# Performance work log

Measured on AMD Instinct MI355X. Metric: run time of the kernel, lower is better.

The kernel has to match this reference:

```python
import jax, jax.numpy as jnp
import numpy as np

H = 16  # n_heads

def _rmsnorm(x, g, eps=1e-6):
    return x * jax.lax.rsqrt(jnp.mean(x * x, axis=-1, keepdims=True) + eps) * g

def _rope_diag(L, hd, dtype):
    # Diagonal of the full [L, hd, hd] rotary matrix: cos(pos * theta_pair) at every dim.
    # (The torch einsum 'bhld,ldd->bhld' extracts this diagonal, so no pairwise rotation occurs.)
    pair = jnp.arange(hd) // 2
    theta = 10000.0 ** (-2.0 * pair / hd)
    return jnp.cos(jnp.arange(L)[:, None].astype(jnp.float32) * theta[None, :]).astype(dtype)


def setup_inputs() -> dict:
    key = jax.random.key(0)
    ks = jax.random.split(key, 8)
    B, L, E = 2, 2048, 2048
    F = 2 * E  # SwiGLU width
    s = 0.02
    return {
        "x": jax.random.normal(ks[0], (B, L, E), jnp.float32),
        "g": jnp.ones((E,), jnp.float32),
        "wq": jax.random.normal(ks[1], (E, E), jnp.float32) * s,
        "wk": jax.random.normal(ks[2], (E, E), jnp.float32) * s,
        "wv": jax.random.normal(ks[3], (E, E), jnp.float32) * s,
        "w1": jax.random.normal(ks[4], (E, F), jnp.float32) * s,
        "b1": jnp.zeros((F,), jnp.float32),
        "wg": jax.random.normal(ks[5], (F, F), jnp.float32) * s,
        "bg": jnp.zeros((F,), jnp.float32),
        "wl": jax.random.normal(ks[6], (F, F), jnp.float32) * s,
        "bl": jnp.zeros((F,), jnp.float32),
        "beta": jnp.ones((1,), jnp.float32),
        "w2": jax.random.normal(ks[7], (F, E), jnp.float32) * s,
        "b2": jnp.zeros((E,), jnp.float32),
    }


def reference(x, g, wq, wk, wv, w1, b1, wg, bg, wl, bl, beta, w2, b2):
    B, L, E = x.shape
    hd = E // H
    x_res = x
    h = _rmsnorm(x, g)
    # projections -> [B, H, L, hd]
    q = (h @ wq).reshape(B, L, H, hd).transpose(0, 2, 1, 3)
    k = (h @ wk).reshape(B, L, H, hd).transpose(0, 2, 1, 3)
    v = (h @ wv).reshape(B, L, H, hd).transpose(0, 2, 1, 3)
    D = _rope_diag(L, hd, x.dtype)  # [L, hd], diagonal of rotary matrix
    q = q * D
    k = k * D
    score = jnp.einsum('bhld,bhmd->bhlm', q, k)  # [B,H,L,L]
    # causal mask added BEFORE scaling (faithful to source)
    mask = jnp.triu(jnp.full((L, L), -jnp.inf, dtype=score.dtype), k=1)
    score = (score + mask) / jnp.sqrt(jnp.asarray(hd, score.dtype))
    attn = jax.nn.softmax(score, axis=-1)
    o = jnp.einsum('bhlm,bhmd->bhld', attn, v)
    o = o.transpose(0, 2, 1, 3).reshape(B, L, E)
    x = o + x_res
    x_res = x
    h = _rmsnorm(x, g)
    h = h @ w1 + b1  # [B, L, 2E]
    gate = h @ wg + bg
    lin = h @ wl + bl
    act = gate * jax.nn.sigmoid(beta * gate) * lin
    out = act @ w2 + b2
    return out + x_res
```

## Files before the change

kernel.cpp:

```cpp
#include <hip/hip_runtime.h>
#include <cstdint>
#include <math.h>


typedef _Float16 f16;
typedef _Float16 f16x8 __attribute__((ext_vector_type(8)));
typedef _Float16 f16x4 __attribute__((ext_vector_type(4)));
typedef float    f32x4 __attribute__((ext_vector_type(4)));

#define MFMA_16x16x32(a, b, c) __builtin_amdgcn_mfma_f32_16x16x32_f16(a, b, c, 0, 0, 0)

__device__ __forceinline__ void gload_lds16(const void* g, void* lds) {
  __builtin_amdgcn_global_load_lds(
      (__attribute__((address_space(1))) void*)(uintptr_t)g,
      (__attribute__((address_space(3))) void*)(unsigned)(uintptr_t)lds,
      16, 0, 0);
}

__global__ void convT_k(const float* __restrict__ W, f16* __restrict__ Wt,
                        int K, int N) {
  __shared__ float tile[32][33];
  const int n0 = blockIdx.x << 5, k0 = blockIdx.y << 5;
  const int t = threadIdx.x;
  const int r = t >> 3, c4 = (t & 7) << 2;
  const f32x4 v = *(const f32x4*)(W + (size_t)(k0 + r) * N + n0 + c4);
  tile[r][c4 + 0] = v[0]; tile[r][c4 + 1] = v[1];
  tile[r][c4 + 2] = v[2]; tile[r][c4 + 3] = v[3];
  __syncthreads();
  f16x4 o;
  o[0] = (f16)tile[c4 + 0][r]; o[1] = (f16)tile[c4 + 1][r];
  o[2] = (f16)tile[c4 + 2][r]; o[3] = (f16)tile[c4 + 3][r];
  *(f16x4*)(Wt + (size_t)(n0 + r) * K + k0 + c4) = o;
}

__global__ void rope_tab_k(float* __restrict__ Dt) {
  const int l = blockIdx.x, d = threadIdx.x;
  const float th = __expf(-0.0719557841f * (float)(d & ~1));
  Dt[(l << 7) + d] = cosf((float)l * th);
}

__global__ void rmsnorm_k(const float* __restrict__ X, const float* __restrict__ G,
                          f16* __restrict__ H) {
  __shared__ float red[4];
  const int row = blockIdx.x, t = threadIdx.x;
  const float* xp = X + ((size_t)row << 11) + (t << 3);
  const f32x4 v0 = *(const f32x4*)xp;
  const f32x4 v1 = *(const f32x4*)(xp + 4);
  float ss = v0[0]*v0[0] + v0[1]*v0[1] + v0[2]*v0[2] + v0[3]*v0[3]
           + v1[0]*v1[0] + v1[1]*v1[1] + v1[2]*v1[2] + v1[3]*v1[3];
#pragma unroll
  for (int m = 1; m < 64; m <<= 1) ss += __shfl_xor(ss, m);
  if ((t & 63) == 0) red[t >> 6] = ss;
  __syncthreads();
  const float tot = red[0] + red[1] + red[2] + red[3];
  const float rs = rsqrtf(tot * (1.f / 2048.f) + 1e-6f);
  const float* gp = G + (t << 3);
  const f32x4 g0 = *(const f32x4*)gp, g1 = *(const f32x4*)(gp + 4);
  f16x8 o;
  o[0] = (f16)(v0[0]*rs*g0[0]); o[1] = (f16)(v0[1]*rs*g0[1]);
  o[2] = (f16)(v0[2]*rs*g0[2]); o[3] = (f16)(v0[3]*rs*g0[3]);
  o[4] = (f16)(v1[0]*rs*g1[0]); o[5] = (f16)(v1[1]*rs*g1[1]);
  o[6] = (f16)(v1[2]*rs*g1[2]); o[7] = (f16)(v1[3]*rs*g1[3]);
  *(f16x8*)(H + ((size_t)row << 11) + (t << 3)) = o;
}

__global__ void vtrans_k(const f16* __restrict__ V, f16* __restrict__ Vt) {
  __shared__ f16 tile[32][36];
  const int l0 = blockIdx.x << 5, d0 = blockIdx.y << 5, bh = blockIdx.z;
  const int b = bh >> 4, h = bh & 15;
  const int t = threadIdx.x;
  const int r = t >> 3, c4 = (t & 7) << 2;
  const f16x4 v = *(const f16x4*)(V + (size_t)((b << 11) + l0 + r) * 2048 + (h << 7) + d0 + c4);
  tile[r][c4 + 0] = v[0]; tile[r][c4 + 1] = v[1];
  tile[r][c4 + 2] = v[2]; tile[r][c4 + 3] = v[3];
  __syncthreads();
  f16x4 o;
  o[0] = tile[c4 + 0][r]; o[1] = tile[c4 + 1][r];
  o[2] = tile[c4 + 2][r]; o[3] = tile[c4 + 3][r];
  *(f16x4*)(Vt + (size_t)((bh << 7) + d0 + r) * 2048 + l0 + c4) = o;
}

template <int EPI>
__launch_bounds__(512, 2)
__global__ void gemm256_k(const f16* __restrict__ A, const f16* __restrict__ Bt,
                          void* __restrict__ Cout, int M, int N, int K,
                          const float* __restrict__ bias,
                          const f16* __restrict__ auxh,
                          const float* __restrict__ betap) {
  __shared__ alignas(16) f16 lds[65536];
  const int t = threadIdx.x, lane = t & 63, w = t >> 6;
  const int wm = w >> 2, wn = w & 3;
  const int bm = blockIdx.y << 8, bn = blockIdx.x << 8;
  const int lh = lane & 15, lq = lane >> 4;
  const int NT = K >> 6;
  const int lrow = lane >> 3;
  const int lco  = ((lane & 7) ^ lrow) << 3;

  const f16* Agl = A  + (size_t)(bm + lrow) * K + lco;
  const f16* Bgl = Bt + (size_t)(bn + lrow) * K + lco;
  const int aw = w << 3;
  const int bw = w << 4;

  f32x4 acc[8][4] = {};
  f16x8 bf[4][2];

  auto stA = [&](int tile, int half) {
    const int d = (tile & 1) << 15;
    const int k0 = tile << 6;
    const int r0 = aw + (half << 6);
    gload_lds16(Agl + (size_t)r0 * K + k0, (void*)&lds[d + r0 * 64]);
    gload_lds16(Agl + (size_t)(r0 + 128) * K + k0, (void*)&lds[d + (r0 + 128) * 64]);
  };
  auto stB = [&](int tile, int half) {
    const int d = ((tile & 1) << 15) + 16384;
    const int k0 = tile << 6;
    const int r0 = bw + (half << 7);
    gload_lds16(Bgl + (size_t)r0 * K + k0, (void*)&lds[d + r0 * 64]);
    gload_lds16(Bgl + (size_t)(r0 + 8) * K + k0, (void*)&lds[d + (r0 + 8) * 64]);
  };
  auto ldA = [&](int d, int mi, int kk) {
    const int r = (wm << 7) + (mi << 4) + lh;
    return *(const f16x8*)&lds[(d << 15) + r * 64 + ((((kk << 2) + lq) ^ (lh & 7)) << 3)];
  };
  auto ldB = [&](int d, int ni, int kk) {
    const int r = (wn << 6) + (ni << 4) + lh;
    return *(const f16x8*)&lds[(d << 15) + 16384 + r * 64 + ((((kk << 2) + lq) ^ (lh & 7)) << 3)];
  };

  stB(0, 0); stB(0, 1); stA(0, 0); stA(0, 1);
  stB(1, 0); stB(1, 1); stA(1, 0);
  asm volatile("s_waitcnt vmcnt(6)" ::: "memory");
  __builtin_amdgcn_s_barrier();

  for (int tt = 0; tt < NT; tt += 2) {
    const bool pf = (tt + 2 < NT);
#pragma unroll
    for (int hf = 0; hf < 2; ++hf) {
#pragma unroll
      for (int ph = 0; ph < 4; ++ph) {
        f16x8 a0k0 = ldA(hf, 2 * ph, 0),     a0k1 = ldA(hf, 2 * ph, 1);
        f16x8 a1k0 = ldA(hf, 2 * ph + 1, 0), a1k1 = ldA(hf, 2 * ph + 1, 1);
        if (ph == 0) {
#pragma unroll
          for (int ni = 0; ni < 4; ++ni) {
            bf[ni][0] = ldB(hf, ni, 0); bf[ni][1] = ldB(hf, ni, 1);
          }
        }
        if (hf == 0) {
          if (ph == 0) stA(tt + 1, 1);
          else if (ph == 1) { if (pf) stB(tt + 2, 0); }
          else if (ph == 2) { if (pf) stB(tt + 2, 1); }
          else              { if (pf) stA(tt + 2, 0); }
        } else {
          if (ph == 0)      { if (pf) stA(tt + 2, 1); }
          else if (ph == 1) { if (pf) stB(tt + 3, 0); }
          else if (ph == 2) { if (pf) stB(tt + 3, 1); }
          else              { if (pf) stA(tt + 3, 0); }
        }
        __builtin_amdgcn_s_barrier();
        __builtin_amdgcn_s_setprio(1);
#pragma unroll
        for (int ni = 0; ni < 4; ++ni) {
          acc[2 * ph][ni]     = MFMA_16x16x32(a0k0, bf[ni][0], acc[2 * ph][ni]);
          acc[2 * ph][ni]     = MFMA_16x16x32(a0k1, bf[ni][1], acc[2 * ph][ni]);
          acc[2 * ph + 1][ni] = MFMA_16x16x32(a1k0, bf[ni][0], acc[2 * ph + 1][ni]);
          acc[2 * ph + 1][ni] = MFMA_16x16x32(a1k1, bf[ni][1], acc[2 * ph + 1][ni]);
        }
        __builtin_amdgcn_s_setprio(0);
        if (ph == 3) {
          if (hf == 0) {
            if (pf) asm volatile("s_waitcnt vmcnt(6)" ::: "memory");
            else    asm volatile("s_waitcnt vmcnt(0)" ::: "memory");
          } else if (pf) {
            asm volatile("s_waitcnt vmcnt(6)" ::: "memory");
          }
        }
        __builtin_amdgcn_s_barrier();
      }
    }
  }

  const float be = (EPI == 3) ? betap[0] : 0.f;
#pragma unroll
  for (int mi = 0; mi < 8; ++mi) {
#pragma unroll
    for (int ni = 0; ni < 4; ++ni) {
#pragma unroll
      for (int r = 0; r < 4; ++r) {
        const int grow = bm + (wm << 7) + (mi << 4) + (lq << 2) + r;
        const int gcol = bn + (wn << 6) + (ni << 4) + lh;
        float v = acc[mi][ni][r] + bias[gcol];
        const size_t off = (size_t)grow * N + gcol;
        if (EPI == 2) {
          ((f16*)Cout)[off] = (f16)v;
        } else if (EPI == 3) {
          ((f16*)Cout)[off] = (f16)(v / (1.f + __expf(-be * v)));
        } else {
          ((f16*)Cout)[off] = (f16)(v * (float)auxh[off]);
        }
      }
    }
  }
}

template <int EPI>
__launch_bounds__(256, 2)
__global__ void gemm_k(const f16* __restrict__ A, const f16* __restrict__ Bt,
                       void* __restrict__ Cout, int M, int N, int K,
                       const float* __restrict__ bias,
                       const float* __restrict__ auxf,
                       float scale) {
  __shared__ alignas(16) f16 As[128 * 64];
  __shared__ alignas(16) f16 Bs[128 * 64];
  const int t = threadIdx.x;
  const int lane = t & 63;
  const int w = t >> 6;
  const int wm = w >> 1, wn = w & 1;
  const int bm = blockIdx.y << 7;
  const int bn = blockIdx.x << 7;
  const int lh = lane & 15, lq = lane >> 4;

  f32x4 acc[4][4] = {};

  for (int k0 = 0; k0 < K; k0 += 64) {
    __syncthreads();
#pragma unroll
    for (int i = 0; i < 4; ++i) {
      const int idx = i * 256 + (w << 6) + lane;
      const int row = idx >> 3, c = idx & 7;
      const int cs = (c ^ (row & 7)) << 3;
      gload_lds16(A + (size_t)(bm + row) * K + k0 + cs,
                  &As[(i * 256 + (w << 6)) << 3]);
      gload_lds16(Bt + (size_t)(bn + row) * K + k0 + cs,
                  &Bs[(i * 256 + (w << 6)) << 3]);
    }
    asm volatile("s_waitcnt vmcnt(0)" ::: "memory");
    __syncthreads();
#pragma unroll
    for (int kk = 0; kk < 2; ++kk) {
      f16x8 af[4], bfr[4];
#pragma unroll
      for (int mi = 0; mi < 4; ++mi) {
        const int r = (wm << 6) + (mi << 4) + lh;
        af[mi] = *(const f16x8*)&As[(r << 6) + ((((kk << 2) + lq) ^ (r & 7)) << 3)];
      }
#pragma unroll
      for (int ni = 0; ni < 4; ++ni) {
        const int r = (wn << 6) + (ni << 4) + lh;
        bfr[ni] = *(const f16x8*)&Bs[(r << 6) + ((((kk << 2) + lq) ^ (r & 7)) << 3)];
      }
#pragma unroll
      for (int mi = 0; mi < 4; ++mi)
#pragma unroll
        for (int ni = 0; ni < 4; ++ni)
          acc[mi][ni] = MFMA_16x16x32(af[mi], bfr[ni], acc[mi][ni]);
    }
  }

#pragma unroll
  for (int mi = 0; mi < 4; ++mi) {
#pragma unroll
    for (int ni = 0; ni < 4; ++ni) {
#pragma unroll
      for (int r = 0; r < 4; ++r) {
        const int grow = bm + (wm << 6) + (mi << 4) + (lq << 2) + r;
        const int gcol = bn + (wn << 6) + (ni << 4) + lh;
        float v = acc[mi][ni][r];
        const size_t off = (size_t)grow * N + gcol;
        if (EPI == 0) {
          v *= scale * auxf[((grow & 2047) << 7) + (gcol & 127)];
          ((f16*)Cout)[off] = (f16)v;
        } else if (EPI == 1) {
          ((f16*)Cout)[off] = (f16)v;
        } else {
          ((float*)Cout)[off] = v + bias[gcol] + auxf[off];
        }
      }
    }
  }
}

__launch_bounds__(256, 2)
__global__ void attn_k(const f16* __restrict__ Q, const f16* __restrict__ Kb,
                       const f16* __restrict__ Vt, const float* __restrict__ Xres,
                       float* __restrict__ X2, int* __restrict__ qcnt) {
  constexpr int L = 2048, E = 2048, HD = 128;
  __shared__ alignas(16) f16 Ks[64 * 128];
  __shared__ alignas(16) f16 Vs[128 * 64];
  __shared__ alignas(16) f16 Ps[4][32 * 72];
  __shared__ int s_item;

  const int t = threadIdx.x, lane = t & 63, w = t >> 6;
  const int lh = lane & 15, lq = lane >> 4;

  for (;;) {
    if (t == 0) s_item = atomicAdd(qcnt, 1);
    __syncthreads();
    const int item = s_item;
    if (item >= 512) return;
    const int bh = item & 31;
    const int q0 = (15 - (item >> 5)) << 7;
    const int b = bh >> 4, h = bh & 15;
    const int wrow0 = q0 + (w << 5);

    f16x8 qf[2][4];
#pragma unroll
    for (int mi = 0; mi < 2; ++mi) {
      const f16* qrow = Q + (size_t)(b * L + wrow0 + (mi << 4) + lh) * E + h * HD;
#pragma unroll
      for (int kq = 0; kq < 4; ++kq)
        qf[mi][kq] = *(const f16x8*)(qrow + (kq << 5) + (lq << 3));
    }

    f32x4 oacc[2][8] = {};
    float mrun[2][4], lrun[2][4];
#pragma unroll
    for (int mi = 0; mi < 2; ++mi)
#pragma unroll
      for (int r = 0; r < 4; ++r) { mrun[mi][r] = -1e30f; lrun[mi][r] = 0.f; }

    const int nkv = q0 + 128;
    for (int kv0 = 0; kv0 < nkv; kv0 += 64) {
      __syncthreads();
#pragma unroll
      for (int i = 0; i < 4; ++i) {
        const int idx = i * 256 + (w << 6) + lane;
        {
          const int row = idx >> 4, c = idx & 15;
          gload_lds16(Kb + (size_t)(b * L + kv0 + row) * E + h * HD + ((c ^ (row & 7)) << 3),
                      &Ks[(i * 256 + (w << 6)) << 3]);
        }
        {
          const int row = idx >> 3, c = idx & 7;
          gload_lds16(Vt + ((size_t)bh * HD + row) * L + kv0 + ((c ^ (row & 7)) << 3),
                      &Vs[(i * 256 + (w << 6)) << 3]);
        }
      }
      asm volatile("s_waitcnt vmcnt(0)" ::: "memory");
      __syncthreads();

      if (kv0 <= wrow0 + 31) {
        f32x4 sacc[2][4] = {};
#pragma unroll
        for (int kq = 0; kq < 4; ++kq) {
          f16x8 kf[4];
#pragma unroll
          for (int ni = 0; ni < 4; ++ni) {
            const int r = (ni << 4) + lh;
            kf[ni] = *(const f16x8*)&Ks[(r << 7) + ((((kq << 2) + lq) ^ (r & 7)) << 3)];
          }
#pragma unroll
          for (int mi = 0; mi < 2; ++mi)
#pragma unroll
            for (int ni = 0; ni < 4; ++ni)
              sacc[mi][ni] = MFMA_16x16x32(qf[mi][kq], kf[ni], sacc[mi][ni]);
        }
        if (kv0 + 63 > wrow0) {
#pragma unroll
          for (int mi = 0; mi < 2; ++mi)
#pragma unroll
            for (int ni = 0; ni < 4; ++ni)
#pragma unroll
              for (int r = 0; r < 4; ++r) {
                const int qr = wrow0 + (mi << 4) + (lq << 2) + r;
                const int kv = kv0 + (ni << 4) + lh;
                if (kv > qr) sacc[mi][ni][r] = -1e30f;
              }
        }
        float scl[2][4], rsum[2][4];
#pragma unroll
        for (int mi = 0; mi < 2; ++mi)
#pragma unroll
          for (int r = 0; r < 4; ++r) {
            float v = fmaxf(fmaxf(sacc[mi][0][r], sacc[mi][1][r]),
                            fmaxf(sacc[mi][2][r], sacc[mi][3][r]));
            v = fmaxf(v, __shfl_xor(v, 1));
            v = fmaxf(v, __shfl_xor(v, 2));
            v = fmaxf(v, __shfl_xor(v, 4));
            v = fmaxf(v, __shfl_xor(v, 8));
            const float mnew = fmaxf(mrun[mi][r], v);
            scl[mi][r] = __expf(mrun[mi][r] - mnew);
            mrun[mi][r] = mnew;
            rsum[mi][r] = 0.f;
          }
#pragma unroll
        for (int mi = 0; mi < 2; ++mi)
#pragma unroll
          for (int ni = 0; ni < 4; ++ni)
#pragma unroll
            for (int r = 0; r < 4; ++r) {
              const float p = __expf(sacc[mi][ni][r] - mrun[mi][r]);
              rsum[mi][r] += p;
              Ps[w][((mi << 4) + (lq << 2) + r) * 72 + (ni << 4) + lh] = (f16)p;
            }
#pragma unroll
        for (int mi = 0; mi < 2; ++mi)
#pragma unroll
          for (int r = 0; r < 4; ++r) {
            float s = rsum[mi][r];
            s += __shfl_xor(s, 1);
            s += __shfl_xor(s, 2);
            s += __shfl_xor(s, 4);
            s += __shfl_xor(s, 8);
            lrun[mi][r] = lrun[mi][r] * scl[mi][r] + s;
          }
#pragma unroll
        for (int mi = 0; mi < 2; ++mi)
#pragma unroll
          for (int nd = 0; nd < 8; ++nd)
#pragma unroll
            for (int r = 0; r < 4; ++r) oacc[mi][nd][r] *= scl[mi][r];
#pragma unroll
        for (int kp = 0; kp < 2; ++kp) {
          f16x8 pf[2];
#pragma unroll
          for (int mi = 0; mi < 2; ++mi)
            pf[mi] = *(const f16x8*)&Ps[w][((mi << 4) + lh) * 72 + (kp << 5) + (lq << 3)];
#pragma unroll
          for (int nd = 0; nd < 8; ++nd) {
            const int r = (nd << 4) + lh;
            const f16x8 vf = *(const f16x8*)&Vs[(r << 6) + ((((kp << 2) + lq) ^ (r & 7)) << 3)];
#pragma unroll
            for (int mi = 0; mi < 2; ++mi)
              oacc[mi][nd] = MFMA_16x16x32(pf[mi], vf, oacc[mi][nd]);
          }
        }
      }
    }
#pragma unroll
    for (int mi = 0; mi < 2; ++mi)
#pragma unroll
      for (int nd = 0; nd < 8; ++nd)
#pragma unroll
        for (int r = 0; r < 4; ++r) {
          const int qr = wrow0 + (mi << 4) + (lq << 2) + r;
          const size_t off = (size_t)(b * L + qr) * E + h * HD + (nd << 4) + lh;
          X2[off] = oacc[mi][nd][r] / lrun[mi][r] + Xres[off];
        }
  }
}

extern "C" void kernel_launch(void* const* d_in, const int* in_sizes, int n_in,
                              void* d_out, int out_size, void* d_ws, size_t ws_size,
                              hipStream_t stream) {
  const float* x    = (const float*)d_in[0];
  const float* g    = (const float*)d_in[1];
  const float* wq   = (const float*)d_in[2];
  const float* wk   = (const float*)d_in[3];
  const float* wv   = (const float*)d_in[4];
  const float* w1   = (const float*)d_in[5];
  const float* b1   = (const float*)d_in[6];
  const float* wgp  = (const float*)d_in[7];
  const float* bg   = (const float*)d_in[8];
  const float* wl   = (const float*)d_in[9];
  const float* bl   = (const float*)d_in[10];
  const float* beta = (const float*)d_in[11];
  const float* w2   = (const float*)d_in[12];
  const float* b2   = (const float*)d_in[13];

  constexpr size_t MB = 1ull << 20;
  char* ws = (char*)d_ws;
  f16*   wT   = (f16*)(ws + 0 * MB);
  int*   qcnt = (int*)(ws + 31 * MB);
  float* Dt   = (float*)(ws + 32 * MB);
  f16*   hbuf = (f16*)(ws + 33 * MB);
  f16*   qbuf = (f16*)(ws + 49 * MB);
  f16*   kbuf = (f16*)(ws + 65 * MB);
  f16*   vbuf = (f16*)(ws + 81 * MB);
  f16*   vtb  = (f16*)(ws + 97 * MB);
  float* x2   = (float*)(ws + 113 * MB);
  f16*   a1   = (f16*)(ws + 49 * MB);
  f16*   sbuf = (f16*)(ws + 81 * MB);
  f16*   act  = (f16*)(ws + 145 * MB);
  (void)ws_size; (void)n_in; (void)in_sizes; (void)out_size;

  const dim3 blk(256);
  const float qscale = 0.08838834764831845f;

  rope_tab_k<<<2048, 128, 0, stream>>>(Dt);
  rmsnorm_k<<<4096, blk, 0, stream>>>(x, g, hbuf);
  hipMemsetAsync(qcnt, 0, 4, stream);

  f16* wqT = wT;
  f16* wkT = wT + (size_t)2048 * 2048;
  f16* wvT = wT + (size_t)4096 * 2048;
  convT_k<<<dim3(64, 64), blk, 0, stream>>>(wq, wqT, 2048, 2048);
  convT_k<<<dim3(64, 64), blk, 0, stream>>>(wk, wkT, 2048, 2048);
  convT_k<<<dim3(64, 64), blk, 0, stream>>>(wv, wvT, 2048, 2048);
  gemm_k<0><<<dim3(16, 32), blk, 0, stream>>>(hbuf, wqT, qbuf, 4096, 2048, 2048,
                                              nullptr, Dt, qscale);
  gemm_k<0><<<dim3(16, 32), blk, 0, stream>>>(hbuf, wkT, kbuf, 4096, 2048, 2048,
                                              nullptr, Dt, 1.0f);
  gemm_k<1><<<dim3(16, 32), blk, 0, stream>>>(hbuf, wvT, vbuf, 4096, 2048, 2048,
                                              nullptr, nullptr, 1.0f);
  vtrans_k<<<dim3(64, 4, 32), blk, 0, stream>>>(vbuf, vtb);

  attn_k<<<384, blk, 0, stream>>>(qbuf, kbuf, vtb, x, x2, qcnt);

  rmsnorm_k<<<4096, blk, 0, stream>>>(x2, g, hbuf);

  convT_k<<<dim3(128, 64), blk, 0, stream>>>(w1, wT, 2048, 4096);
  gemm256_k<2><<<dim3(16, 16), 512, 0, stream>>>(hbuf, wT, a1, 4096, 4096, 2048,
                                                 b1, nullptr, nullptr);
  convT_k<<<dim3(128, 128), blk, 0, stream>>>(wgp, wT, 4096, 4096);
  gemm256_k<3><<<dim3(16, 16), 512, 0, stream>>>(a1, wT, sbuf, 4096, 4096, 4096,
                                                 bg, nullptr, beta);
  convT_k<<<dim3(128, 128), blk, 0, stream>>>(wl, wT, 4096, 4096);
  gemm256_k<4><<<dim3(16, 16), 512, 0, stream>>>(a1, wT, act, 4096, 4096, 4096,
                                                 bl, sbuf, nullptr);
  convT_k<<<dim3(64, 128), blk, 0, stream>>>(w2, wT, 4096, 2048);
  gemm_k<5><<<dim3(16, 32), blk, 0, stream>>>(act, wT, (float*)d_out, 4096, 2048, 4096,
                                              b2, x2, 1.0f);
}
```

Measured before the change: 728.5 us.

## Software-pipeline LDS fragment loads one phase ahead of MFMA in GEMM

Double-buffers the A and B register fragments so each phase issues the LDS reads for the next phase before running the current MFMAs. The loads for the next K half-tile are hoisted into phase 3, and the vmcnt wait moves to just before those reads with a tighter count. The aim is to hide LDS read latency behind matrix instructions. In exchange the kernel holds more fragment registers, which may cut occupancy, and the barrier and waitcnt placement is more delicate to get right.

```diff
diff --git a/kernel.cpp b/kernel.cpp
--- a/kernel.cpp
+++ b/kernel.cpp
@@ -102,7 +102,8 @@
   const int bw = w << 4;
 
   f32x4 acc[8][4] = {};
-  f16x8 bf[4][2];
+  f16x8 aset[2][4];
+  f16x8 bset[2][4][2];
 
   auto stA = [&](int tile, int half) {
     const int d = (tile & 1) << 15;
@@ -126,11 +127,26 @@
     const int r = (wn << 6) + (ni << 4) + lh;
     return *(const f16x8*)&lds[(d << 15) + 16384 + r * 64 + ((((kk << 2) + lq) ^ (lh & 7)) << 3)];
   };
+  auto ldAq = [&](int buf, int q, int par) {
+    aset[par][0] = ldA(buf, 2 * q, 0);
+    aset[par][1] = ldA(buf, 2 * q, 1);
+    aset[par][2] = ldA(buf, 2 * q + 1, 0);
+    aset[par][3] = ldA(buf, 2 * q + 1, 1);
+  };
+  auto ldBt = [&](int buf) {
+#pragma unroll
+    for (int ni = 0; ni < 4; ++ni) {
+      bset[buf][ni][0] = ldB(buf, ni, 0);
+      bset[buf][ni][1] = ldB(buf, ni, 1);
+    }
+  };
 
   stB(0, 0); stB(0, 1); stA(0, 0); stA(0, 1);
   stB(1, 0); stB(1, 1); stA(1, 0);
   asm volatile("s_waitcnt vmcnt(6)" ::: "memory");
   __builtin_amdgcn_s_barrier();
+  ldAq(0, 0, 0);
+  ldBt(0);
 
   for (int tt = 0; tt < NT; tt += 2) {
     const bool pf = (tt + 2 < NT);
@@ -138,13 +154,18 @@
     for (int hf = 0; hf < 2; ++hf) {
 #pragma unroll
       for (int ph = 0; ph < 4; ++ph) {
-        f16x8 a0k0 = ldA(hf, 2 * ph, 0),     a0k1 = ldA(hf, 2 * ph, 1);
-        f16x8 a1k0 = ldA(hf, 2 * ph + 1, 0), a1k1 = ldA(hf, 2 * ph + 1, 1);
-        if (ph == 0) {
-#pragma unroll
-          for (int ni = 0; ni < 4; ++ni) {
-            bf[ni][0] = ldB(hf, ni, 0); bf[ni][1] = ldB(hf, ni, 1);
-          }
+        const int cur = ph & 1, nxt = (ph + 1) & 1;
+        if (ph < 3) {
+          ldAq(hf, ph + 1, nxt);
+        } else if (hf == 0) {
+          if (pf) asm volatile("s_waitcnt vmcnt(4)" ::: "memory");
+          else    asm volatile("s_waitcnt vmcnt(0)" ::: "memory");
+          ldAq(1, 0, nxt);
+          ldBt(1);
+        } else if (pf) {
+          asm volatile("s_waitcnt vmcnt(4)" ::: "memory");
+          ldAq(0, 0, nxt);
+          ldBt(0);
         }
         if (hf == 0) {
           if (ph == 0) stA(tt + 1, 1);
@@ -161,20 +182,12 @@
         __builtin_amdgcn_s_setprio(1);
 #pragma unroll
         for (int ni = 0; ni < 4; ++ni) {
-          acc[2 * ph][ni]     = MFMA_16x16x32(a0k0, bf[ni][0], acc[2 * ph][ni]);
-          acc[2 * ph][ni]     = MFMA_16x16x32(a0k1, bf[ni][1], acc[2 * ph][ni]);
-          acc[2 * ph + 1][ni] = MFMA_16x16x32(a1k0, bf[ni][0], acc[2 * ph + 1][ni]);
-          acc[2 * ph + 1][ni] = MFMA_16x16x32(a1k1, bf[ni][1], acc[2 * ph + 1][ni]);
+          acc[2 * ph][ni]     = MFMA_16x16x32(aset[cur][0], bset[hf][ni][0], acc[2 * ph][ni]);
+          acc[2 * ph][ni]     = MFMA_16x16x32(aset[cur][1], bset[hf][ni][1], acc[2 * ph][ni]);
+          acc[2 * ph + 1][ni] = MFMA_16x16x32(aset[cur][2], bset[hf][ni][0], acc[2 * ph + 1][ni]);
+          acc[2 * ph + 1][ni] = MFMA_16x16x32(aset[cur][3], bset[hf][ni][1], acc[2 * ph + 1][ni]);
         }
         __builtin_amdgcn_s_setprio(0);
-        if (ph == 3) {
-          if (hf == 0) {
-            if (pf) asm volatile("s_waitcnt vmcnt(6)" ::: "memory");
-            else    asm volatile("s_waitcnt vmcnt(0)" ::: "memory");
-          } else if (pf) {
-            asm volatile("s_waitcnt vmcnt(6)" ::: "memory");
-          }
-        }
         __builtin_amdgcn_s_barrier();
       }
     }
```

Result: slower. 1.368 ms (+87.8%).

## Double-buffer K tiles and overlap V loads with QK softmax in attention

Applied to the files above, without the earlier changes.

The attention kernel now keeps two K tile buffers in LDS and prefetches the next K tile while the current one is consumed. The V tile load is issued at the start of each iteration and only waited on before the PV MFMA, so it overlaps with the QK^T and softmax work. This hides global-to-LDS latency that was previously fully exposed, at the cost of extra LDS (possibly lower occupancy), an extra barrier per iteration, and fragile hand-counted vmcnt waits.

```diff
diff --git a/kernel.cpp b/kernel.cpp
--- a/kernel.cpp
+++ b/kernel.cpp
@@ -285,7 +285,7 @@
                        const f16* __restrict__ Vt, const float* __restrict__ Xres,
                        float* __restrict__ X2, int* __restrict__ qcnt) {
   constexpr int L = 2048, E = 2048, HD = 128;
-  __shared__ alignas(16) f16 Ks[64 * 128];
+  __shared__ alignas(16) f16 Ks[2][64 * 128];
   __shared__ alignas(16) f16 Vs[128 * 64];
   __shared__ alignas(16) f16 Ps[4][32 * 72];
   __shared__ int s_item;
@@ -303,6 +303,25 @@
     const int b = bh >> 4, h = bh & 15;
     const int wrow0 = q0 + (w << 5);
 
+    auto issueK = [&](int kv0, int buf) {
+#pragma unroll
+      for (int i = 0; i < 4; ++i) {
+        const int idx = i * 256 + (w << 6) + lane;
+        const int row = idx >> 4, c = idx & 15;
+        gload_lds16(Kb + (size_t)(b * L + kv0 + row) * E + h * HD + ((c ^ (row & 7)) << 3),
+                    &Ks[buf][(i * 256 + (w << 6)) << 3]);
+      }
+    };
+    auto issueV = [&](int kv0) {
+#pragma unroll
+      for (int i = 0; i < 4; ++i) {
+        const int idx = i * 256 + (w << 6) + lane;
+        const int row = idx >> 3, c = idx & 7;
+        gload_lds16(Vt + ((size_t)bh * HD + row) * L + kv0 + ((c ^ (row & 7)) << 3),
+                    &Vs[(i * 256 + (w << 6)) << 3]);
+      }
+    };
+
     f16x8 qf[2][4];
 #pragma unroll
     for (int mi = 0; mi < 2; ++mi) {
@@ -311,6 +330,7 @@
       for (int kq = 0; kq < 4; ++kq)
         qf[mi][kq] = *(const f16x8*)(qrow + (kq << 5) + (lq << 3));
     }
+    asm volatile("s_waitcnt vmcnt(0)" ::: "memory");
 
     f32x4 oacc[2][8] = {};
     float mrun[2][4], lrun[2][4];
@@ -319,27 +339,23 @@
 #pragma unroll
       for (int r = 0; r < 4; ++r) { mrun[mi][r] = -1e30f; lrun[mi][r] = 0.f; }
 
-    const int nkv = q0 + 128;
-    for (int kv0 = 0; kv0 < nkv; kv0 += 64) {
-      __syncthreads();
-#pragma unroll
-      for (int i = 0; i < 4; ++i) {
-        const int idx = i * 256 + (w << 6) + lane;
-        {
-          const int row = idx >> 4, c = idx & 15;
-          gload_lds16(Kb + (size_t)(b * L + kv0 + row) * E + h * HD + ((c ^ (row & 7)) << 3),
-                      &Ks[(i * 256 + (w << 6)) << 3]);
-        }
-        {
-          const int row = idx >> 3, c = idx & 7;
-          gload_lds16(Vt + ((size_t)bh * HD + row) * L + kv0 + ((c ^ (row & 7)) << 3),
-                      &Vs[(i * 256 + (w << 6)) << 3]);
-        }
-      }
-      asm volatile("s_waitcnt vmcnt(0)" ::: "memory");
-      __syncthreads();
-
-      if (kv0 <= wrow0 + 31) {
+    const int nt = (q0 + 128) >> 6;
+    issueK(0, 0);
+    for (int it = 0; it < nt; ++it) {
+      const int cur = it & 1;
+      const int kv0 = it << 6;
+      const bool more = (it + 1 < nt);
+      issueV(kv0);
+      if (more) {
+        issueK(kv0 + 64, cur ^ 1);
+        asm volatile("s_waitcnt vmcnt(8)" ::: "memory");
+      } else {
+        asm volatile("s_waitcnt vmcnt(4)" ::: "memory");
+      }
+      __builtin_amdgcn_s_barrier();
+
+      const bool active = (kv0 <= wrow0 + 31);
+      if (active) {
         f32x4 sacc[2][4] = {};
 #pragma unroll
         for (int kq = 0; kq < 4; ++kq) {
@@ -347,7 +363,7 @@
 #pragma unroll
           for (int ni = 0; ni < 4; ++ni) {
             const int r = (ni << 4) + lh;
-            kf[ni] = *(const f16x8*)&Ks[(r << 7) + ((((kq << 2) + lq) ^ (r & 7)) << 3)];
+            kf[ni] = *(const f16x8*)&Ks[cur][(r << 7) + ((((kq << 2) + lq) ^ (r & 7)) << 3)];
           }
 #pragma unroll
           for (int mi = 0; mi < 2; ++mi)
@@ -410,6 +426,13 @@
           for (int nd = 0; nd < 8; ++nd)
 #pragma unroll
             for (int r = 0; r < 4; ++r) oacc[mi][nd][r] *= scl[mi][r];
+      }
+
+      if (more) asm volatile("s_waitcnt vmcnt(4)" ::: "memory");
+      else      asm volatile("s_waitcnt vmcnt(0)" ::: "memory");
+      __builtin_amdgcn_s_barrier();
+
+      if (active) {
 #pragma unroll
         for (int kp = 0; kp < 2; ++kp) {
           f16x8 pf[2];
@@ -426,6 +449,8 @@
           }
         }
       }
+      asm volatile("" ::: "memory");
+      __builtin_amdgcn_s_barrier();
     }
 #pragma unroll
     for (int mi = 0; mi < 2; ++mi)
```

After: 727.1 us. About the same (-0.2%).
